# Kernel tuning notes

Measured on AMD Instinct MI355X. Metric: run time of the kernel, lower is better.

Reference implementation:

```python
import jax, jax.numpy as jnp
import numpy as np
import math

B, S, D, H = 2, 2048, 1024, 16
DQ = D // H  # d_qkv = 64


def setup_inputs() -> dict:
    key = jax.random.key(0)
    k1, k2, k3, k4 = jax.random.split(key, 4)
    return {
        "Q": jax.random.normal(k1, (B, S, D), dtype=jnp.float32),
        "K": jax.random.normal(k2, (B, S, D), dtype=jnp.float32),
        "V": jax.random.normal(k3, (B, S, D), dtype=jnp.float32),
        "Wo_w": jax.random.normal(k4, (D, D), dtype=jnp.float32) * 0.02,
        "Wo_b": jnp.zeros((D,), dtype=jnp.float32),
        "mask": 1,
    }


def reference(Q, K, V, Wo_w, Wo_b, mask):
    # Note: original module defines Wq/Wk/Wv but never applies them in forward.
    q = Q.reshape(B, S, H, DQ)
    k = K.reshape(B, S, H, DQ)
    v = V.reshape(B, S, H, DQ)
    # raw QK^T scores: [B, H, S, S]
    scores = jnp.einsum("bqhd,bkhd->bhqk", q, k)
    if mask:
        # torch.triu_indices(S, S) default offset=0 -> mask where key >= query
        # (diagonal included). Fill applied BEFORE the sqrt(d) scaling, as in source.
        tri = jnp.arange(S)[:, None] <= jnp.arange(S)[None, :]  # [S, S]
        scores = jnp.where(tri, jnp.float32(-1e9), scores)
    scale = scores / math.sqrt(DQ)
    attn = jax.nn.softmax(scale, axis=-1)
    ctx = jnp.einsum("bhqk,bkhd->bqhd", attn, v).reshape(B, S, D)
    return ctx @ Wo_w.T + Wo_b
```

## Files before the change

### kernel.cpp

```cpp
#include <hip/hip_runtime.h>
#include <hip/hip_bf16.h>
#include <stdint.h>

#define B_  2
#define S_  2048
#define D_  1024
#define H_  16
#define DQ_ 64
#define QT_ (S_/64)
#define EXPC1_ 0.18033688f
#define EXPC2_ (-23.083121f)

typedef float f32x4 __attribute__((ext_vector_type(4)));
typedef short bf16x8 __attribute__((ext_vector_type(8)));

__device__ __forceinline__ unsigned short f2bf(float f) {
    uint32_t u = __float_as_uint(f);
    u += 0x7fffu + ((u >> 16) & 1u);
    return (unsigned short)(u >> 16);
}
__device__ __forceinline__ float bf2f(unsigned short u) {
    return __uint_as_float(((uint32_t)u) << 16);
}
__device__ __forceinline__ bf16x8 packbf8(float4 a, float4 b) {
    bf16x8 r;
    r[0]=(short)f2bf(a.x); r[1]=(short)f2bf(a.y);
    r[2]=(short)f2bf(a.z); r[3]=(short)f2bf(a.w);
    r[4]=(short)f2bf(b.x); r[5]=(short)f2bf(b.y);
    r[6]=(short)f2bf(b.z); r[7]=(short)f2bf(b.w);
    return r;
}

__global__ __launch_bounds__(256) void prep_kernel(
    const float* __restrict__ K, const float* __restrict__ V,
    const float* __restrict__ W,
    unsigned short* __restrict__ Kb, unsigned short* __restrict__ Vt,
    unsigned short* __restrict__ Wb, float* __restrict__ Pv)
{
    __shared__ unsigned short Ls[64][72];
    const int blk = blockIdx.x, tid = threadIdx.x;

    if (blk < 1024) {
        const int st = blk & 31, h = (blk >> 5) & 15, b = blk >> 9;
        {
            int row = tid >> 2, col0 = (tid & 3) * 16;
            const float* src = V + (((size_t)b*S_ + (size_t)st*64 + row)*D_ + h*64 + col0);
            float4 f0 = ((const float4*)src)[0];
            float4 f1 = ((const float4*)src)[1];
            float4 f2 = ((const float4*)src)[2];
            float4 f3 = ((const float4*)src)[3];
            unsigned short* d = &Ls[row][col0];
            d[0]=f2bf(f0.x); d[1]=f2bf(f0.y); d[2]=f2bf(f0.z); d[3]=f2bf(f0.w);
            d[4]=f2bf(f1.x); d[5]=f2bf(f1.y); d[6]=f2bf(f1.z); d[7]=f2bf(f1.w);
            d[8]=f2bf(f2.x); d[9]=f2bf(f2.y); d[10]=f2bf(f2.z); d[11]=f2bf(f2.w);
            d[12]=f2bf(f3.x); d[13]=f2bf(f3.y); d[14]=f2bf(f3.z); d[15]=f2bf(f3.w);
        }
        __syncthreads();
        {
            int d = tid >> 2, scol = (tid & 3) * 16;
            unsigned short tmp[16];
            float psum = 0.f;
            #pragma unroll
            for (int i = 0; i < 16; ++i) {
                unsigned short u = Ls[scol + i][d];
                tmp[i] = u;
                psum += bf2f(u);
            }
            unsigned short* dst = Vt + ((size_t)((b*H_ + h)*64 + d)*S_ + st*64 + scol);
            ((uint4*)dst)[0] = *((uint4*)tmp);
            ((uint4*)dst)[1] = *((uint4*)(tmp + 8));
            psum += __shfl_xor(psum, 1);
            psum += __shfl_xor(psum, 2);
            if ((tid & 3) == 0)
                Pv[((size_t)(b*H_ + h)*64 + d)*32 + st] = psum;
        }
    } else if (blk < 5120) {
        int i = (blk - 1024)*256 + tid;
        float4 f = ((const float4*)K)[i];
        ushort4 o;
        o.x = f2bf(f.x); o.y = f2bf(f.y); o.z = f2bf(f.z); o.w = f2bf(f.w);
        ((ushort4*)Kb)[i] = o;
    } else {
        int i = (blk - 5120)*256 + tid;
        float4 f = ((const float4*)W)[i];
        ushort4 o;
        o.x = f2bf(f.x); o.y = f2bf(f.y); o.z = f2bf(f.z); o.w = f2bf(f.w);
        ((ushort4*)Wb)[i] = o;
    }
}

__global__ __launch_bounds__(256, 2) void attn_kernel(
    const float* __restrict__ Q,
    const unsigned short* __restrict__ Kb,
    const unsigned short* __restrict__ Vtb,
    const float* __restrict__ Pv,
    unsigned short* __restrict__ ctx,
    const int* __restrict__ maskp)
{
    __shared__ unsigned short Ks [2][64][72];
    __shared__ unsigned short Vts[2][64][72];
    __shared__ unsigned short Ps [4][32][72];

    const int bid = blockIdx.x;
    const int g = bid & 31, pp = bid >> 5;
    const int h = g & 15, b = g >> 4;
    const int tid  = threadIdx.x;
    const int wave = tid >> 6, lane = tid & 63;
    const int quad = lane >> 4, ln = lane & 15;
    const int maskv = maskp[0];

    if (maskv && pp == 0 && tid < 64) {
        const float* p = Pv + ((size_t)(b*H_ + h)*64 + tid)*32;
        float s = 0.f;
        #pragma unroll
        for (int i = 0; i < 32; ++i) s += p[i];
        ctx[(size_t)b*S_*D_ + h*64 + tid] = f2bf(s * (1.0f/S_));
    }

    const int srow = tid >> 2, scol = (tid & 3)*16;
    const unsigned short* kbase =
        Kb + (((size_t)b*S_ + srow)*D_ + h*64 + scol);
    const unsigned short* vbase =
        Vtb + ((size_t)((b*H_ + h)*64 + srow)*S_ + scol);

    for (int t = 0; t < 2; ++t) {
        const int grp = t ? (15 - pp) : pp;
        const int niter = maskv ? (2*grp + 2) : QT_;
        const int qw0 = grp*128 + wave*32;

        bf16x8 bq[2][2];
        #pragma unroll
        for (int qt2 = 0; qt2 < 2; ++qt2) {
            const float* qr = Q + (((size_t)b*S_ + qw0 + qt2*16 + ln)*D_
                                   + h*64 + quad*8);
            #pragma unroll
            for (int dqs = 0; dqs < 2; ++dqs) {
                float4 f0 = ((const float4*)(qr + dqs*32))[0];
                float4 f1 = ((const float4*)(qr + dqs*32))[1];
                bq[qt2][dqs] = packbf8(f0, f1);
            }
        }

        uint4 k0 = ((const uint4*)kbase)[0], k1 = ((const uint4*)kbase)[1];
        uint4 v0 = ((const uint4*)vbase)[0], v1 = ((const uint4*)vbase)[1];

        f32x4 o[2][4] = {};
        float l4[2] = {0.f, 0.f};

        if (t) __syncthreads();

        for (int j = 0; j < niter; ++j) {
            const int cur = j & 1;
            *((uint4*)&Ks [cur][srow][scol])   = k0;
            *((uint4*)&Ks [cur][srow][scol+8]) = k1;
            *((uint4*)&Vts[cur][srow][scol])   = v0;
            *((uint4*)&Vts[cur][srow][scol+8]) = v1;
            if (j + 1 < niter) {
                const unsigned short* kp = kbase + (size_t)(j+1)*64*D_;
                const unsigned short* vp = vbase + (j+1)*64;
                k0 = ((const uint4*)kp)[0]; k1 = ((const uint4*)kp)[1];
                v0 = ((const uint4*)vp)[0]; v1 = ((const uint4*)vp)[1];
            }
            __syncthreads();

            if (maskv && j*64 >= qw0 + 32) continue;

            f32x4 s[4][2] = {};
            #pragma unroll
            for (int dqs = 0; dqs < 2; ++dqs)
                #pragma unroll
                for (int kt = 0; kt < 4; ++kt) {
                    bf16x8 aK = *(const bf16x8*)&Ks[cur][kt*16 + ln][dqs*32 + quad*8];
                    #pragma unroll
                    for (int qt2 = 0; qt2 < 2; ++qt2)
                        s[kt][qt2] = __builtin_amdgcn_mfma_f32_16x16x32_bf16(
                            aK, bq[qt2][dqs], s[kt][qt2], 0,0,0);
                }

            const int needmask = maskv && (j*64 + 63 >= qw0);
            #pragma unroll
            for (int qt2 = 0; qt2 < 2; ++qt2) {
                const int qgl = qw0 + qt2*16 + ln;
                #pragma unroll
                for (int kt = 0; kt < 4; ++kt) {
                    const int kg = j*64 + kt*16 + quad*4;
                    float e[4];
                    #pragma unroll
                    for (int r = 0; r < 4; ++r) {
                        float v = exp2f(fmaf(s[kt][qt2][r], EXPC1_, EXPC2_));
                        if (needmask && (kg + r) >= qgl) v = 0.f;
                        e[r] = v;
                    }
                    l4[qt2] += (e[0] + e[1]) + (e[2] + e[3]);
                    uint2 w;
                    w.x = ((uint32_t)f2bf(e[1]) << 16) | f2bf(e[0]);
                    w.y = ((uint32_t)f2bf(e[3]) << 16) | f2bf(e[2]);
                    *((uint2*)&Ps[wave][qt2*16 + ln][kt*16 + quad*4]) = w;
                }
            }

            bf16x8 ap[2][2];
            #pragma unroll
            for (int qt2 = 0; qt2 < 2; ++qt2)
                #pragma unroll
                for (int ks2 = 0; ks2 < 2; ++ks2)
                    ap[qt2][ks2] = *(const bf16x8*)&Ps[wave][qt2*16 + ln][ks2*32 + quad*8];
            #pragma unroll
            for (int ks2 = 0; ks2 < 2; ++ks2)
                #pragma unroll
                for (int dd = 0; dd < 4; ++dd) {
                    bf16x8 bv = *(const bf16x8*)&Vts[cur][dd*16 + ln][ks2*32 + quad*8];
                    #pragma unroll
                    for (int qt2 = 0; qt2 < 2; ++qt2)
                        o[qt2][dd] = __builtin_amdgcn_mfma_f32_16x16x32_bf16(
                            ap[qt2][ks2], bv, o[qt2][dd], 0,0,0);
                }
        }

        #pragma unroll
        for (int qt2 = 0; qt2 < 2; ++qt2) {
            l4[qt2] += __shfl_xor(l4[qt2], 16);
            l4[qt2] += __shfl_xor(l4[qt2], 32);
        }
        float inv[2][4];
        #pragma unroll
        for (int qt2 = 0; qt2 < 2; ++qt2)
            #pragma unroll
            for (int r = 0; r < 4; ++r)
                inv[qt2][r] = 1.0f / __shfl(l4[qt2], quad*4 + r);
        #pragma unroll
        for (int qt2 = 0; qt2 < 2; ++qt2)
            #pragma unroll
            for (int dd = 0; dd < 4; ++dd)
                #pragma unroll
                for (int r = 0; r < 4; ++r) {
                    int q = qw0 + qt2*16 + quad*4 + r;
                    if (maskv && q == 0) continue;
                    int c = h*64 + dd*16 + ln;
                    ctx[((size_t)b*S_ + q)*D_ + c] = f2bf(o[qt2][dd][r]*inv[qt2][r]);
                }
        __syncthreads();
    }
}

__global__ __launch_bounds__(256, 2) void proj_kernel(
    const unsigned short* __restrict__ A,
    const unsigned short* __restrict__ Bw,
    const float* __restrict__ bias,
    float* __restrict__ out)
{
    __shared__ unsigned short As[2][64][72];
    __shared__ unsigned short Bs[2][128][72];
    const int nt0 = blockIdx.x;
    const int mt0 = blockIdx.y;
    const int tid  = threadIdx.x;
    const int wave = tid >> 6, lane = tid & 63;
    const int quad = lane >> 4, ln = lane & 15;

    const int arow = tid >> 2, acol = (tid & 3)*16;
    const int brow = tid >> 1, bcol = (tid & 1)*32;
    const unsigned short* aptr = A  + ((size_t)(mt0*64  + arow)*1024 + acol);
    const unsigned short* bptr = Bw + ((size_t)(nt0*128 + brow)*1024 + bcol);

    uint4 a0 = ((const uint4*)aptr)[0], a1 = ((const uint4*)aptr)[1];
    uint4 b0 = ((const uint4*)bptr)[0], b1 = ((const uint4*)bptr)[1],
          b2 = ((const uint4*)bptr)[2], b3 = ((const uint4*)bptr)[3];

    f32x4 acc[4][2] = {};

    for (int kt = 0; kt < 16; ++kt) {
        const int cur = kt & 1;
        *((uint4*)&As[cur][arow][acol])    = a0;
        *((uint4*)&As[cur][arow][acol+8])  = a1;
        *((uint4*)&Bs[cur][brow][bcol])    = b0;
        *((uint4*)&Bs[cur][brow][bcol+8])  = b1;
        *((uint4*)&Bs[cur][brow][bcol+16]) = b2;
        *((uint4*)&Bs[cur][brow][bcol+24]) = b3;
        uint4 na0, na1, nb0, nb1, nb2, nb3;
        if (kt < 15) {
            const unsigned short* ap = aptr + (kt+1)*64;
            const unsigned short* bp = bptr + (kt+1)*64;
            na0 = ((const uint4*)ap)[0]; na1 = ((const uint4*)ap)[1];
            nb0 = ((const uint4*)bp)[0]; nb1 = ((const uint4*)bp)[1];
            nb2 = ((const uint4*)bp)[2]; nb3 = ((const uint4*)bp)[3];
        }
        __syncthreads();
        #pragma unroll
        for (int ks = 0; ks < 2; ++ks) {
            bf16x8 am[4], bn[2];
            #pragma unroll
            for (int i = 0; i < 4; ++i)
                am[i] = *(const bf16x8*)&As[cur][i*16 + ln][ks*32 + quad*8];
            #pragma unroll
            for (int i = 0; i < 2; ++i)
                bn[i] = *(const bf16x8*)&Bs[cur][wave*32 + i*16 + ln][ks*32 + quad*8];
            #pragma unroll
            for (int mi = 0; mi < 4; ++mi)
                #pragma unroll
                for (int ni = 0; ni < 2; ++ni)
                    acc[mi][ni] = __builtin_amdgcn_mfma_f32_16x16x32_bf16(
                        am[mi], bn[ni], acc[mi][ni], 0,0,0);
        }
        a0 = na0; a1 = na1;
        b0 = nb0; b1 = nb1; b2 = nb2; b3 = nb3;
    }

    #pragma unroll
    for (int mi = 0; mi < 4; ++mi)
        #pragma unroll
        for (int ni = 0; ni < 2; ++ni) {
            int row = mt0*64 + mi*16 + quad*4;
            int col = nt0*128 + wave*32 + ni*16 + ln;
            float bv = bias[col];
            #pragma unroll
            for (int r = 0; r < 4; ++r)
                out[(size_t)(row + r)*1024 + col] = acc[mi][ni][r] + bv;
        }
}

extern "C" void kernel_launch(void* const* d_in, const int* in_sizes, int n_in,
                              void* d_out, int out_size, void* d_ws, size_t ws_size,
                              hipStream_t stream)
{
    const float* Q   = (const float*)d_in[0];
    const float* K   = (const float*)d_in[1];
    const float* V   = (const float*)d_in[2];
    const float* Wo  = (const float*)d_in[3];
    const float* Wb  = (const float*)d_in[4];
    const int* maskp = (const int*)d_in[5];
    float* out = (float*)d_out;

    unsigned short* Kb   = (unsigned short*)d_ws;
    unsigned short* Vtb  = Kb  + (size_t)B_*S_*D_;
    unsigned short* Wob  = Vtb + (size_t)B_*S_*D_;
    unsigned short* ctxb = Wob + (size_t)D_*D_;
    float* Pv = (float*)(ctxb + (size_t)B_*S_*D_);

    prep_kernel<<<6144, 256, 0, stream>>>(K, V, Wo, Kb, Vtb, Wob, Pv);
    attn_kernel<<<512/2, 256, 0, stream>>>(Q, Kb, Vtb, Pv, ctxb, maskp);
    proj_kernel<<<dim3(8, 64), 256, 0, stream>>>(ctxb, Wob, Wb, out);
}
```

Baseline: 175.9 us.

## Split attention key range across two blocks and combine partials in reduce kernel

Each (batch, head, query-group pair) now runs as two blocks, each covering half of the key tiles. Unnormalized bf16 partial outputs and row sums go to workspace, and a new reduce kernel sums them, normalizes, and writes ctx, including the special row 0. This doubles the attention grid from 256 to 512 blocks to fill more CUs. The cost is an extra kernel launch and extra partial-result traffic. The probability packing also switches from round-to-nearest to truncation via a byte-permute, which saves ALU work but adds a small bias.

Result: slower. 184.8 us (+5.0%).

```diff
diff --git a/kernel.cpp b/kernel.cpp
--- a/kernel.cpp
+++ b/kernel.cpp
@@ -29,6 +29,10 @@
     r[4]=(short)f2bf(b.x); r[5]=(short)f2bf(b.y);
     r[6]=(short)f2bf(b.z); r[7]=(short)f2bf(b.w);
     return r;
+}
+__device__ __forceinline__ uint32_t packtrunc(float hi, float lo) {
+    return __builtin_amdgcn_perm(__float_as_uint(hi), __float_as_uint(lo),
+                                 0x07060302u);
 }
 
 __global__ __launch_bounds__(256) void prep_kernel(
@@ -93,8 +97,8 @@
     const float* __restrict__ Q,
     const unsigned short* __restrict__ Kb,
     const unsigned short* __restrict__ Vtb,
-    const float* __restrict__ Pv,
-    unsigned short* __restrict__ ctx,
+    unsigned short* __restrict__ Opart,
+    float* __restrict__ lpart,
     const int* __restrict__ maskp)
 {
     __shared__ unsigned short Ks [2][64][72];
@@ -102,20 +106,13 @@
     __shared__ unsigned short Ps [4][32][72];
 
     const int bid = blockIdx.x;
-    const int g = bid & 31, pp = bid >> 5;
-    const int h = g & 15, b = g >> 4;
+    const int bh = bid & 31, sc = bid >> 5;
+    const int pp = sc >> 1, c = sc & 1;
+    const int h = bh & 15, b = bh >> 4;
     const int tid  = threadIdx.x;
     const int wave = tid >> 6, lane = tid & 63;
     const int quad = lane >> 4, ln = lane & 15;
     const int maskv = maskp[0];
-
-    if (maskv && pp == 0 && tid < 64) {
-        const float* p = Pv + ((size_t)(b*H_ + h)*64 + tid)*32;
-        float s = 0.f;
-        #pragma unroll
-        for (int i = 0; i < 32; ++i) s += p[i];
-        ctx[(size_t)b*S_*D_ + h*64 + tid] = f2bf(s * (1.0f/S_));
-    }
 
     const int srow = tid >> 2, scol = (tid & 3)*16;
     const unsigned short* kbase =
@@ -124,9 +121,10 @@
         Vtb + ((size_t)((b*H_ + h)*64 + srow)*S_ + scol);
 
     for (int t = 0; t < 2; ++t) {
-        const int grp = t ? (15 - pp) : pp;
-        const int niter = maskv ? (2*grp + 2) : QT_;
-        const int qw0 = grp*128 + wave*32;
+        const int g = t ? (15 - pp) : pp;
+        const int n = maskv ? (2*g + 2) : QT_;
+        const int j0 = (c*n) >> 1, j1 = ((c+1)*n) >> 1;
+        const int qw0 = g*128 + wave*32;
 
         bf16x8 bq[2][2];
         #pragma unroll
@@ -141,21 +139,23 @@
             }
         }
 
-        uint4 k0 = ((const uint4*)kbase)[0], k1 = ((const uint4*)kbase)[1];
-        uint4 v0 = ((const uint4*)vbase)[0], v1 = ((const uint4*)vbase)[1];
+        uint4 k0 = ((const uint4*)(kbase + (size_t)j0*64*D_))[0];
+        uint4 k1 = ((const uint4*)(kbase + (size_t)j0*64*D_))[1];
+        uint4 v0 = ((const uint4*)(vbase + j0*64))[0];
+        uint4 v1 = ((const uint4*)(vbase + j0*64))[1];
 
         f32x4 o[2][4] = {};
         float l4[2] = {0.f, 0.f};
 
         if (t) __syncthreads();
 
-        for (int j = 0; j < niter; ++j) {
+        for (int j = j0; j < j1; ++j) {
             const int cur = j & 1;
             *((uint4*)&Ks [cur][srow][scol])   = k0;
             *((uint4*)&Ks [cur][srow][scol+8]) = k1;
             *((uint4*)&Vts[cur][srow][scol])   = v0;
             *((uint4*)&Vts[cur][srow][scol+8]) = v1;
-            if (j + 1 < niter) {
+            if (j + 1 < j1) {
                 const unsigned short* kp = kbase + (size_t)(j+1)*64*D_;
                 const unsigned short* vp = vbase + (j+1)*64;
                 k0 = ((const uint4*)kp)[0]; k1 = ((const uint4*)kp)[1];
@@ -193,8 +193,8 @@
                     }
                     l4[qt2] += (e[0] + e[1]) + (e[2] + e[3]);
                     uint2 w;
-                    w.x = ((uint32_t)f2bf(e[1]) << 16) | f2bf(e[0]);
-                    w.y = ((uint32_t)f2bf(e[3]) << 16) | f2bf(e[2]);
+                    w.x = packtrunc(e[1], e[0]);
+                    w.y = packtrunc(e[3], e[2]);
                     *((uint2*)&Ps[wave][qt2*16 + ln][kt*16 + quad*4]) = w;
                 }
             }
@@ -222,25 +222,83 @@
             l4[qt2] += __shfl_xor(l4[qt2], 16);
             l4[qt2] += __shfl_xor(l4[qt2], 32);
         }
-        float inv[2][4];
+        const size_t slot = (size_t)bh*32 + g*2 + c;
+        if (quad == 0) {
+            #pragma unroll
+            for (int qt2 = 0; qt2 < 2; ++qt2)
+                lpart[slot*128 + wave*32 + qt2*16 + ln] = l4[qt2];
+        }
+        unsigned short* ob = Opart + slot*(128*64);
         #pragma unroll
         for (int qt2 = 0; qt2 < 2; ++qt2)
             #pragma unroll
-            for (int r = 0; r < 4; ++r)
-                inv[qt2][r] = 1.0f / __shfl(l4[qt2], quad*4 + r);
-        #pragma unroll
-        for (int qt2 = 0; qt2 < 2; ++qt2)
-            #pragma unroll
             for (int dd = 0; dd < 4; ++dd)
                 #pragma unroll
                 for (int r = 0; r < 4; ++r) {
-                    int q = qw0 + qt2*16 + quad*4 + r;
-                    if (maskv && q == 0) continue;
-                    int c = h*64 + dd*16 + ln;
-                    ctx[((size_t)b*S_ + q)*D_ + c] = f2bf(o[qt2][dd][r]*inv[qt2][r]);
+                    int q8 = wave*32 + qt2*16 + quad*4 + r;
+                    int dq = dd*16 + ln;
+                    ob[q8*64 + dq] = f2bf(o[qt2][dd][r]);
                 }
         __syncthreads();
     }
+}
+
+__global__ __launch_bounds__(256) void reduce_kernel(
+    const unsigned short* __restrict__ Opart,
+    const float* __restrict__ lpart,
+    const float* __restrict__ Pv,
+    unsigned short* __restrict__ ctx,
+    const int* __restrict__ maskp)
+{
+    const int blk = blockIdx.x;
+    const int bh = blk >> 4, g = blk & 15;
+    const int h = bh & 15, b = bh >> 4;
+    const int tid = threadIdx.x;
+    const int q = tid >> 1, dq0 = (tid & 1)*32;
+    const int gq = g*128 + q;
+    const int maskv = maskp[0];
+
+    unsigned short outv[32];
+    if (maskv && gq == 0) {
+        #pragma unroll 4
+        for (int i = 0; i < 32; ++i) {
+            const float* p = Pv + ((size_t)bh*64 + dq0 + i)*32;
+            float s = 0.f;
+            #pragma unroll
+            for (int k = 0; k < 32; ++k) s += p[k];
+            outv[i] = f2bf(s * (1.0f/S_));
+        }
+    } else {
+        float acc[32];
+        #pragma unroll
+        for (int i = 0; i < 32; ++i) acc[i] = 0.f;
+        float l = 0.f;
+        const size_t slot0 = (size_t)bh*32 + g*2;
+        #pragma unroll
+        for (int c = 0; c < 2; ++c) {
+            const unsigned short* op = Opart + (slot0 + c)*(128*64) + q*64 + dq0;
+            #pragma unroll
+            for (int u = 0; u < 4; ++u) {
+                uint4 v = ((const uint4*)op)[u];
+                acc[u*8+0] += bf2f((unsigned short)(v.x & 0xffff));
+                acc[u*8+1] += bf2f((unsigned short)(v.x >> 16));
+                acc[u*8+2] += bf2f((unsigned short)(v.y & 0xffff));
+                acc[u*8+3] += bf2f((unsigned short)(v.y >> 16));
+                acc[u*8+4] += bf2f((unsigned short)(v.z & 0xffff));
+                acc[u*8+5] += bf2f((unsigned short)(v.z >> 16));
+                acc[u*8+6] += bf2f((unsigned short)(v.w & 0xffff));
+                acc[u*8+7] += bf2f((unsigned short)(v.w >> 16));
+            }
+            l += lpart[(slot0 + c)*128 + q];
+        }
+        float inv = 1.0f / l;
+        #pragma unroll
+        for (int i = 0; i < 32; ++i) outv[i] = f2bf(acc[i]*inv);
+    }
+    unsigned short* dst = ctx + ((size_t)b*S_ + gq)*D_ + h*64 + dq0;
+    #pragma unroll
+    for (int u = 0; u < 4; ++u)
+        ((uint4*)dst)[u] = ((uint4*)outv)[u];
 }
 
 __global__ __launch_bounds__(256, 2) void proj_kernel(
@@ -331,12 +389,15 @@
     float* out = (float*)d_out;
 
     unsigned short* Kb   = (unsigned short*)d_ws;
-    unsigned short* Vtb  = Kb  + (size_t)B_*S_*D_;
-    unsigned short* Wob  = Vtb + (size_t)B_*S_*D_;
-    unsigned short* ctxb = Wob + (size_t)D_*D_;
-    float* Pv = (float*)(ctxb + (size_t)B_*S_*D_);
+    unsigned short* Vtb  = Kb   + (size_t)B_*S_*D_;
+    unsigned short* Wob  = Vtb  + (size_t)B_*S_*D_;
+    unsigned short* ctxb = Wob  + (size_t)D_*D_;
+    unsigned short* Opart= ctxb + (size_t)B_*S_*D_;
+    float* lpart = (float*)(Opart + (size_t)32*32*128*64);
+    float* Pv    = lpart + (size_t)32*32*128;
 
     prep_kernel<<<6144, 256, 0, stream>>>(K, V, Wo, Kb, Vtb, Wob, Pv);
-    attn_kernel<<<512/2, 256, 0, stream>>>(Q, Kb, Vtb, Pv, ctxb, maskp);
+    attn_kernel<<<512, 256, 0, stream>>>(Q, Kb, Vtb, Opart, lpart, maskp);
+    reduce_kernel<<<512, 256, 0, stream>>>(Opart, lpart, Pv, ctxb, maskp);
     proj_kernel<<<dim3(8, 64), 256, 0, stream>>>(ctxb, Wob, Wb, out);
 }
```
